# Kernel optimization log

Measured on AMD Instinct MI355X. Metric: run time of the kernel, lower is better.

## Reference

```python
import jax, jax.numpy as jnp
import numpy as np

EPS = 1e-6
NH, DK, DV = 4, 32, 32

def _ln2d(x, w, b):
    # LayerNorm2d: normalize over channel dim (dim=1), biased variance
    mu = jnp.mean(x, axis=1, keepdims=True)
    var = jnp.mean((x - mu) ** 2, axis=1, keepdims=True)
    y = (x - mu) / jnp.sqrt(var + EPS)
    return w[None, :, None, None] * y + b[None, :, None, None]

def _c1x1(w, x):
    # 1x1 conv == per-pixel matmul: w [out,in], x [B,C,H,W]
    return jnp.einsum('oc,bchw->bohw', w, x)

def _shifts(x, r):
    # All (2r+1)^2 zero-padded spatial shifts, row-major (dy,dx) like nn.Unfold.
    B, C, H, W = x.shape
    xp = jnp.pad(x, ((0, 0), (0, 0), (r, r), (r, r)))
    return jnp.stack([xp[:, :, dy:dy + H, dx:dx + W]
                      for dy in range(2 * r + 1) for dx in range(2 * r + 1)], axis=0)

def _local_attn(q, k, v, kernel):
    # Correlation-pyramid local attention: per-pixel q.k over kxk window of k,
    # softmax over window (temperature sqrt(d_k)), weighted sum of v window
    # (weights shared across channels, per ChannelAttention).
    B, _, H, W = q.shape
    r = (kernel - 1) // 2
    K2 = kernel * kernel
    qh = q.reshape(B, NH, DK, H, W)
    ks = _shifts(k, r).reshape(K2, B, NH, DK, H, W)
    corr = jnp.einsum('bncyx,jbncyx->jbnyx', qh, ks)            # [K2,B,NH,H,W]
    attn = jax.nn.softmax(corr / jnp.sqrt(jnp.float32(DK)), axis=0)
    vs = _shifts(v, r).reshape(K2, B, NH, DV, H, W)
    out = jnp.einsum('jbnyx,jbncyx->bncyx', attn, vs)
    return out.reshape(B, NH * DV, H, W)

def _mha(q, k, v, kernel, wq, wk, wv, fc, lnw, lnb):
    resid = q
    heads = _local_attn(_c1x1(wq, q), _c1x1(wk, k), _c1x1(wv, v), kernel)
    out = _c1x1(fc, heads) + resid   # residual BEFORE LN (per source)
    return _ln2d(out, lnw, lnb)

def _ffn(x, w1, b1, w2, b2, lnw, lnb):
    h = jax.nn.relu(_c1x1(w1, x) + b1[None, :, None, None])
    y = _c1x1(w2, h) + b2[None, :, None, None]
    return _ln2d(y, lnw, lnb) + x    # LN BEFORE residual add (per source)

def setup_inputs():
    key = jax.random.key(0)
    ks = jax.random.split(key, 24)
    B, C, H, W = 4, 128, 96, 96
    s = (2.0 / C) ** 0.5
    f = jnp.float32
    return {
        'input1': jax.random.normal(ks[0], (B, C, H, W), f),
        'input2': jax.random.normal(ks[1], (B, C, H, W), f),
        'wq_s': jax.random.normal(ks[2], (NH * DK, C), f) * s,
        'wk_s': jax.random.normal(ks[3], (NH * DK, C), f) * s,
        'wv_s': jax.random.normal(ks[4], (NH * DV, C), f) * s,
        'fc_s': jax.random.normal(ks[5], (C, NH * DV), f) * s,
        'lnw_s': jnp.ones((C,), f),
        'lnb_s': jnp.zeros((C,), f),
        'wq_c': jax.random.normal(ks[6], (NH * DK, C), f) * s,
        'wk_c': jax.random.normal(ks[7], (NH * DK, C), f) * s,
        'wv_c': jax.random.normal(ks[8], (NH * DV, C), f) * s,
        'fc_c': jax.random.normal(ks[9], (C, NH * DV), f) * s,
        'lnw_c': jnp.ones((C,), f),
        'lnb_c': jnp.zeros((C,), f),
        'w1': jax.random.normal(ks[10], (C, C), f) * s,
        'b1': jnp.zeros((C,), f),
        'w2': jax.random.normal(ks[11], (C, C), f) * s,
        'b2': jnp.zeros((C,), f),
        'lnw_f': jnp.ones((C,), f),
        'lnb_f': jnp.zeros((C,), f),
        'kernel': 5,
        'pad': 2,
    }

def reference(input1, input2, wq_s, wk_s, wv_s, fc_s, lnw_s, lnb_s,
              wq_c, wk_c, wv_c, fc_c, lnw_c, lnb_c,
              w1, b1, w2, b2, lnw_f, lnb_f, kernel, pad):
    slf1 = _mha(input1, input1, input1, kernel, wq_s, wk_s, wv_s, fc_s, lnw_s, lnb_s)
    slf2 = _mha(input2, input2, input2, kernel, wq_s, wk_s, wv_s, fc_s, lnw_s, lnb_s)
    crs1 = _mha(slf1, slf2, slf2, kernel, wq_c, wk_c, wv_c, fc_c, lnw_c, lnb_c)
    crs2 = _mha(slf2, slf1, slf1, kernel, wq_c, wk_c, wv_c, fc_c, lnw_c, lnb_c)
    out1 = _ffn(crs1, w1, b1, w2, b2, lnw_f, lnb_f)
    out2 = _ffn(crs2, w1, b1, w2, b2, lnw_f, lnb_f)
    return (out1, out2)
```

## Files before the change

kernel.cpp:

```cpp
#include <hip/hip_runtime.h>
#include <hip/hip_bf16.h>

typedef _Float16 h16;
typedef __attribute__((ext_vector_type(8))) _Float16 f16x8v;
typedef __attribute__((ext_vector_type(2))) _Float16 h2v;
typedef __attribute__((ext_vector_type(4))) float f32x4;
#define DI __device__ __forceinline__

constexpr int CH = 128;
constexpr int HH = 96, WW = 96;
constexpr int HW = HH * WW;
constexpr int NB = 4;
constexpr int NPIX = NB * HW;
constexpr int LDT = 136;
constexpr size_t HP = (size_t)NPIX * 32;
constexpr int GH = NPIX / 64;
constexpr int TY = 4, TX = 32;
constexpr int HYH = TY + 4, HXH = TX + 4;
constexpr int LDC = 40;
constexpr int ATB = NPIX / (TY * TX) * 4;

struct __attribute__((aligned(16))) h16x8 { h16 h[8]; };
struct Set { h16 *q, *k, *v; };

DI float h2f(h16 x) { return (float)x; }
DI h16   f2h(float x) { return (h16)x; }


DI void stage_x_cl(const h16* __restrict__ src, int ldx, h16* xl, int t) {
    #pragma unroll
    for (int i = 0; i < 4; ++i) {
        int id = t + 256 * i, px = id >> 4, cc = (id & 15) * 8;
        *reinterpret_cast<f16x8v*>(&xl[px * LDT + cc]) =
            *reinterpret_cast<const f16x8v*>(&src[(size_t)px * ldx + cc]);
    }
}

DI void stage_x_pl(const float* __restrict__ src, h16* xl, int t) {
    #pragma unroll
    for (int i = 0; i < 8; ++i) {
        int id = t + 256 * i, c = id >> 4, p4 = (id & 15) * 4;
        float4 v = *reinterpret_cast<const float4*>(&src[(size_t)c * HW + p4]);
        xl[(p4 + 0) * LDT + c] = f2h(v.x);
        xl[(p4 + 1) * LDT + c] = f2h(v.y);
        xl[(p4 + 2) * LDT + c] = f2h(v.z);
        xl[(p4 + 3) * LDT + c] = f2h(v.w);
    }
}

DI void stage_x_hm(const h16* __restrict__ Tq, h16* xl, int p0, int t) {
    const int px = t >> 2, c8 = (t & 3) * 8;
    #pragma unroll
    for (int h = 0; h < 4; ++h)
        *reinterpret_cast<f16x8v*>(&xl[px * LDT + h * 32 + c8]) =
            *reinterpret_cast<const f16x8v*>(&Tq[(size_t)h * HP + (size_t)(p0 + px) * 32 + c8]);
}

DI void stage_w(const float* __restrict__ w, h16* wl, int t) {
    #pragma unroll
    for (int i = 0; i < 8; ++i) {
        int id = t + 256 * i, o = id >> 4, cc = (id & 15) * 8;
        float4 a = *reinterpret_cast<const float4*>(&w[o * CH + cc]);
        float4 b = *reinterpret_cast<const float4*>(&w[o * CH + cc + 4]);
        h16x8 tmp;
        tmp.h[0] = f2h(a.x); tmp.h[1] = f2h(a.y); tmp.h[2] = f2h(a.z); tmp.h[3] = f2h(a.w);
        tmp.h[4] = f2h(b.x); tmp.h[5] = f2h(b.y); tmp.h[6] = f2h(b.z); tmp.h[7] = f2h(b.w);
        *reinterpret_cast<f16x8v*>(&wl[o * LDT + cc]) = *reinterpret_cast<const f16x8v*>(&tmp);
    }
}

DI void stage_r_pl(const float* __restrict__ src, float* rl, int t) {
    #pragma unroll
    for (int i = 0; i < 8; ++i) {
        int id = t + 256 * i, c = id >> 4, p4 = (id & 15) * 4;
        float4 v = *reinterpret_cast<const float4*>(&src[(size_t)c * HW + p4]);
        rl[c * 65 + p4 + 0] = v.x;
        rl[c * 65 + p4 + 1] = v.y;
        rl[c * 65 + p4 + 2] = v.z;
        rl[c * 65 + p4 + 3] = v.w;
    }
}

DI void gemm64(const h16* xl, const h16* wl, int w, int l, f32x4* acc) {
    const int s = l & 15, g = l >> 4;
    #pragma unroll
    for (int ks = 0; ks < 4; ++ks) {
        f16x8v a = *reinterpret_cast<const f16x8v*>(&xl[(16 * w + s) * LDT + ks * 32 + g * 8]);
        #pragma unroll
        for (int n = 0; n < 8; ++n) {
            f16x8v b = *reinterpret_cast<const f16x8v*>(&wl[(16 * n + s) * LDT + ks * 32 + g * 8]);
            acc[n] = __builtin_amdgcn_mfma_f32_16x16x32_f16(a, b, acc[n], 0, 0, 0);
        }
    }
}

DI void qkv_epi(const f32x4* acc, h16* comp, int p0, int w, int l) {
    const int s = l & 15, g = l >> 4;
    #pragma unroll
    for (int n = 0; n < 8; ++n) {
        const int o = 16 * n + s, head = o >> 5, ch = o & 31;
        h16* pl = comp + (size_t)head * HP;
        #pragma unroll
        for (int j = 0; j < 4; ++j) {
            int px = 16 * w + 4 * g + j;
            pl[(size_t)(p0 + px) * 32 + ch] = f2h(acc[n][j]);
        }
    }
}

DI void ln128(float r[8][4], const float* gm, const float* bt, float val[8][4]) {
    #pragma unroll
    for (int j = 0; j < 4; ++j) {
        float sm = 0.f, sq = 0.f;
        #pragma unroll
        for (int n = 0; n < 8; ++n) { float v = r[n][j]; sm += v; sq += v * v; }
        sm += __shfl_xor(sm, 1); sq += __shfl_xor(sq, 1);
        sm += __shfl_xor(sm, 2); sq += __shfl_xor(sq, 2);
        sm += __shfl_xor(sm, 4); sq += __shfl_xor(sq, 4);
        sm += __shfl_xor(sm, 8); sq += __shfl_xor(sq, 8);
        const float mu = sm * (1.f / 128.f);
        const float var = sq * (1.f / 128.f) - mu * mu;
        const float rs = rsqrtf(var + 1e-6f);
        #pragma unroll
        for (int n = 0; n < 8; ++n)
            val[n][j] = gm[n] * (r[n][j] - mu) * rs + bt[n];
    }
}

__global__ __launch_bounds__(256, 2)
void qkv_self_b(const float* __restrict__ x0, const float* __restrict__ x1,
                const float* __restrict__ w0, const float* __restrict__ w1_,
                const float* __restrict__ w2_, Set sA, Set sB) {
    __shared__ h16 xl[64 * LDT];
    __shared__ h16 wl[CH * LDT];
    const int bid = blockIdx.x, half = bid / GH, p0 = (bid % GH) * 64;
    const float* xv = half ? x1 : x0;
    Set S = half ? sB : sA;
    const int t = threadIdx.x;
    const int b = p0 / HW, hw0 = p0 % HW;
    stage_x_pl(xv + (size_t)b * CH * HW + hw0, xl, t);
    const int w = t >> 6, l = t & 63;
    #pragma unroll
    for (int m = 0; m < 3; ++m) {
        const float* wm = (m == 0) ? w0 : ((m == 1) ? w1_ : w2_);
        h16* comp = (m == 0) ? S.q : ((m == 1) ? S.k : S.v);
        __syncthreads();
        stage_w(wm, wl, t);
        __syncthreads();
        f32x4 acc[8];
        #pragma unroll
        for (int n = 0; n < 8; ++n) acc[n] = {0.f, 0.f, 0.f, 0.f};
        gemm64(xl, wl, w, l, acc);
        qkv_epi(acc, comp, p0, w, l);
    }
}

__global__ __launch_bounds__(256)
void attn5b(Set s0, Set s1) {
    __shared__ h16 kv[HYH * HXH * LDC];
    const int bid = blockIdx.x, setId = bid / ATB, id = bid - setId * ATB;
    Set S = setId ? s1 : s0;
    const int n = id & 3, tile = id >> 2;
    const int img = tile / 72, rem = tile % 72, tr = rem / 3, tc = rem % 3;
    const int y0 = tr * TY, x0 = tc * TX;
    const int t = threadIdx.x;
    const int p = t >> 1, half = t & 1, ch16 = half * 16;
    const int ty = p >> 5, tx = p & 31;
    h16* Qh = S.q + (size_t)n * HP;
    const h16* Kh = S.k + (size_t)n * HP;
    const h16* Vh = S.v + (size_t)n * HP;
    const int gp = img * HW + (y0 + ty) * WW + (x0 + tx);
    h16* qp = Qh + (size_t)gp * 32 + ch16;

    f16x8v q0 = *reinterpret_cast<const f16x8v*>(qp);
    f16x8v q1 = *reinterpret_cast<const f16x8v*>(qp + 8);
    {
        const h16 sc = (h16)0.17677669529663689f;
        #pragma unroll
        for (int e = 0; e < 8; ++e) { q0[e] *= sc; q1[e] *= sc; }
    }

    #pragma unroll
    for (int i = 0; i < 5; ++i) {
        int id2 = t + 256 * i;
        if (id2 < 1152) {
            int r = id2 / 144, c = id2 - r * 144, px = c >> 2, c8 = (c & 3) * 8;
            int y = y0 + r - 2, x = x0 + px - 2;
            f16x8v v = {0, 0, 0, 0, 0, 0, 0, 0};
            if ((unsigned)y < (unsigned)HH && (unsigned)x < (unsigned)WW)
                v = *reinterpret_cast<const f16x8v*>(&Kh[((size_t)(img * HW + y * WW + x)) * 32 + c8]);
            *reinterpret_cast<f16x8v*>(&kv[(r * HXH + px) * LDC + c8]) = v;
        }
    }
    __syncthreads();

    float corr[25];
    #pragma unroll
    for (int dy = 0; dy < 5; ++dy)
        #pragma unroll
        for (int dx = 0; dx < 5; ++dx) {
            const h16* kp = &kv[((ty + dy) * HXH + tx + dx) * LDC + ch16];
            f16x8v k0 = *reinterpret_cast<const f16x8v*>(kp);
            f16x8v k1 = *reinterpret_cast<const f16x8v*>(kp + 8);
            float s;
#if __has_builtin(__builtin_amdgcn_fdot2)
            s = __builtin_amdgcn_fdot2(h2v{q0[0], q0[1]}, h2v{k0[0], k0[1]}, 0.f, false);
            s = __builtin_amdgcn_fdot2(h2v{q0[2], q0[3]}, h2v{k0[2], k0[3]}, s, false);
            s = __builtin_amdgcn_fdot2(h2v{q0[4], q0[5]}, h2v{k0[4], k0[5]}, s, false);
            s = __builtin_amdgcn_fdot2(h2v{q0[6], q0[7]}, h2v{k0[6], k0[7]}, s, false);
            s = __builtin_amdgcn_fdot2(h2v{q1[0], q1[1]}, h2v{k1[0], k1[1]}, s, false);
            s = __builtin_amdgcn_fdot2(h2v{q1[2], q1[3]}, h2v{k1[2], k1[3]}, s, false);
            s = __builtin_amdgcn_fdot2(h2v{q1[4], q1[5]}, h2v{k1[4], k1[5]}, s, false);
            s = __builtin_amdgcn_fdot2(h2v{q1[6], q1[7]}, h2v{k1[6], k1[7]}, s, false);
#else
            s = 0.f;
            #pragma unroll
            for (int e = 0; e < 8; ++e) s += h2f(q0[e]) * h2f(k0[e]);
            #pragma unroll
            for (int e = 0; e < 8; ++e) s += h2f(q1[e]) * h2f(k1[e]);
#endif
            s += __shfl_xor(s, 1);
            corr[dy * 5 + dx] = s;
        }

    float m = corr[0];
    #pragma unroll
    for (int j = 1; j < 25; ++j) m = fmaxf(m, corr[j]);
    float sum = 0.f;
    #pragma unroll
    for (int j = 0; j < 25; ++j) {
        float e = __expf(corr[j] - m);
        corr[j] = e; sum += e;
    }
    const float inv = 1.f / sum;

    __syncthreads();
    #pragma unroll
    for (int i = 0; i < 5; ++i) {
        int id2 = t + 256 * i;
        if (id2 < 1152) {
            int r = id2 / 144, c = id2 - r * 144, px = c >> 2, c8 = (c & 3) * 8;
            int y = y0 + r - 2, x = x0 + px - 2;
            f16x8v v = {0, 0, 0, 0, 0, 0, 0, 0};
            if ((unsigned)y < (unsigned)HH && (unsigned)x < (unsigned)WW)
                v = *reinterpret_cast<const f16x8v*>(&Vh[((size_t)(img * HW + y * WW + x)) * 32 + c8]);
            *reinterpret_cast<f16x8v*>(&kv[(r * HXH + px) * LDC + c8]) = v;
        }
    }
    __syncthreads();

    f16x8v o0 = {0, 0, 0, 0, 0, 0, 0, 0};
    f16x8v o1 = {0, 0, 0, 0, 0, 0, 0, 0};
    #pragma unroll
    for (int dy = 0; dy < 5; ++dy)
        #pragma unroll
        for (int dx = 0; dx < 5; ++dx) {
            const h16 ah = f2h(corr[dy * 5 + dx]);
            const f16x8v av = {ah, ah, ah, ah, ah, ah, ah, ah};
            const h16* vp = &kv[((ty + dy) * HXH + tx + dx) * LDC + ch16];
            f16x8v v0 = *reinterpret_cast<const f16x8v*>(vp);
            f16x8v v1 = *reinterpret_cast<const f16x8v*>(vp + 8);
            o0 += av * v0;
            o1 += av * v1;
        }
    {
        const h16 ih = f2h(inv);
        const f16x8v iv = {ih, ih, ih, ih, ih, ih, ih, ih};
        o0 *= iv; o1 *= iv;
    }
    *reinterpret_cast<f16x8v*>(qp)     = o0;
    *reinterpret_cast<f16x8v*>(qp + 8) = o1;
}

__global__ __launch_bounds__(256, 2)
void fcx1_b(const h16* __restrict__ tA, const h16* __restrict__ tB,
            const float* __restrict__ in1, const float* __restrict__ in2,
            const float* __restrict__ wfc, const float* __restrict__ gamma,
            const float* __restrict__ beta,
            const float* __restrict__ wq, const float* __restrict__ wk,
            const float* __restrict__ wv,
            h16* __restrict__ x1g, h16* __restrict__ x2g, Set c1, Set c2) {
    __shared__ h16 xl[64 * LDT];
    __shared__ __align__(16) char wsm[CH * LDT * 2];
    h16*   wl = (h16*)wsm;
    float* rl = (float*)wsm;
    const int bid = blockIdx.x, half = bid / GH, p0 = (bid % GH) * 64;
    const h16*   tin = half ? tB : tA;
    const float* inr = half ? in2 : in1;
    h16*         xg  = half ? x2g : x1g;
    Set own   = half ? c2 : c1;
    Set other = half ? c1 : c2;
    const int t = threadIdx.x;
    const int w = t >> 6, l = t & 63, s = l & 15, g4 = l >> 4;
    const int b = p0 / HW, hw0 = p0 % HW;

    stage_x_hm(tin, xl, p0, t);
    stage_w(wfc, wl, t);
    __syncthreads();

    f32x4 accF[8];
    #pragma unroll
    for (int n = 0; n < 8; ++n) accF[n] = {0.f, 0.f, 0.f, 0.f};
    gemm64(xl, wl, w, l, accF);
    __syncthreads();

    stage_r_pl(inr + (size_t)b * CH * HW + hw0, rl, t);
    __syncthreads();

    h16 vX[8][4];
    {
        float gm[8], bt[8], r[8][4], val[8][4];
        #pragma unroll
        for (int n = 0; n < 8; ++n) { gm[n] = gamma[16 * n + s]; bt[n] = beta[16 * n + s]; }
        #pragma unroll
        for (int n = 0; n < 8; ++n) {
            const int o = 16 * n + s;
            #pragma unroll
            for (int j = 0; j < 4; ++j) {
                const int px = 16 * w + 4 * g4 + j;
                r[n][j] = accF[n][j] + rl[o * 65 + px];
            }
        }
        ln128(r, gm, bt, val);
        #pragma unroll
        for (int n = 0; n < 8; ++n)
            #pragma unroll
            for (int j = 0; j < 4; ++j) vX[n][j] = f2h(val[n][j]);
    }
    __syncthreads();
    #pragma unroll
    for (int n = 0; n < 8; ++n) {
        const int o = 16 * n + s;
        #pragma unroll
        for (int j = 0; j < 4; ++j) {
            const int px = 16 * w + 4 * g4 + j;
            xl[px * LDT + o] = vX[n][j];
            xg[(size_t)(p0 + px) * CH + o] = vX[n][j];
        }
    }
    stage_w(wq, wl, t);
    __syncthreads();
    {
        f32x4 acc[8];
        #pragma unroll
        for (int n = 0; n < 8; ++n) acc[n] = {0.f, 0.f, 0.f, 0.f};
        gemm64(xl, wl, w, l, acc);
        qkv_epi(acc, own.q, p0, w, l);
    }
    __syncthreads();
    stage_w(wk, wl, t);
    __syncthreads();
    {
        f32x4 acc[8];
        #pragma unroll
        for (int n = 0; n < 8; ++n) acc[n] = {0.f, 0.f, 0.f, 0.f};
        gemm64(xl, wl, w, l, acc);
        qkv_epi(acc, other.k, p0, w, l);
    }
    __syncthreads();
    stage_w(wv, wl, t);
    __syncthreads();
    {
        f32x4 acc[8];
        #pragma unroll
        for (int n = 0; n < 8; ++n) acc[n] = {0.f, 0.f, 0.f, 0.f};
        gemm64(xl, wl, w, l, acc);
        qkv_epi(acc, other.v, p0, w, l);
    }
}

__global__ __launch_bounds__(256, 2)
void ffn_ln_b(const h16* __restrict__ t0, const h16* __restrict__ t1,
              const h16* __restrict__ x0, const h16* __restrict__ x1,
              const float* __restrict__ wfc, const float* __restrict__ gc,
              const float* __restrict__ bc,
              const float* __restrict__ w1m, const float* __restrict__ b1v,
              const float* __restrict__ w2m, const float* __restrict__ b2v,
              const float* __restrict__ gf, const float* __restrict__ bf,
              float* __restrict__ o0, float* __restrict__ o1) {
    __shared__ __align__(16) char smem[64 * LDT * 2 * 2 + CH * LDT * 2];
    h16*   xl = (h16*)smem;
    h16*   yl = (h16*)(smem + 64 * LDT * 2);
    h16*   wl = (h16*)(smem + 64 * LDT * 2 * 2);
    float* ll = (float*)(smem + 64 * LDT * 2 * 2);
    const int bid = blockIdx.x, half = bid / GH, p0 = (bid % GH) * 64;
    const h16* tin = half ? t1 : t0;
    const h16* xg  = half ? x1 : x0;
    float* outp = half ? o1 : o0;
    const int t = threadIdx.x;
    const int w = t >> 6, l = t & 63, s = l & 15, g4 = l >> 4;

    stage_x_hm(tin, xl, p0, t);
    stage_w(wfc, wl, t);
    __syncthreads();

    h16 yv[8][4];
    {
        f32x4 acc[8];
        #pragma unroll
        for (int n = 0; n < 8; ++n) acc[n] = {0.f, 0.f, 0.f, 0.f};
        gemm64(xl, wl, w, l, acc);
        float gm[8], bt[8], r[8][4], val[8][4];
        #pragma unroll
        for (int n = 0; n < 8; ++n) { gm[n] = gc[16 * n + s]; bt[n] = bc[16 * n + s]; }
        #pragma unroll
        for (int n = 0; n < 8; ++n) {
            const int o = 16 * n + s;
            #pragma unroll
            for (int j = 0; j < 4; ++j) {
                const int px = 16 * w + 4 * g4 + j;
                r[n][j] = acc[n][j] + h2f(xg[(size_t)(p0 + px) * CH + o]);
            }
        }
        ln128(r, gm, bt, val);
        #pragma unroll
        for (int n = 0; n < 8; ++n)
            #pragma unroll
            for (int j = 0; j < 4; ++j) yv[n][j] = f2h(val[n][j]);
    }
    __syncthreads();
    #pragma unroll
    for (int n = 0; n < 8; ++n) {
        const int o = 16 * n + s;
        #pragma unroll
        for (int j = 0; j < 4; ++j)
            yl[(16 * w + 4 * g4 + j) * LDT + o] = yv[n][j];
    }
    stage_w(w1m, wl, t);
    __syncthreads();

    {
        f32x4 acc[8];
        #pragma unroll
        for (int n = 0; n < 8; ++n) acc[n] = {0.f, 0.f, 0.f, 0.f};
        gemm64(yl, wl, w, l, acc);
        #pragma unroll
        for (int n = 0; n < 8; ++n) {
            const int o = 16 * n + s;
            const float bv = b1v[o];
            #pragma unroll
            for (int j = 0; j < 4; ++j)
                xl[(16 * w + 4 * g4 + j) * LDT + o] = f2h(fmaxf(acc[n][j] + bv, 0.f));
        }
    }
    __syncthreads();
    stage_w(w2m, wl, t);
    __syncthreads();

    float val[8][4];
    {
        f32x4 acc[8];
        #pragma unroll
        for (int n = 0; n < 8; ++n) acc[n] = {0.f, 0.f, 0.f, 0.f};
        gemm64(xl, wl, w, l, acc);
        float gm[8], bt[8], r[8][4];
        #pragma unroll
        for (int n = 0; n < 8; ++n) { gm[n] = gf[16 * n + s]; bt[n] = bf[16 * n + s]; }
        #pragma unroll
        for (int n = 0; n < 8; ++n) {
            const int o = 16 * n + s;
            const float bv = b2v[o];
            #pragma unroll
            for (int j = 0; j < 4; ++j) r[n][j] = acc[n][j] + bv;
        }
        ln128(r, gm, bt, val);
        #pragma unroll
        for (int n = 0; n < 8; ++n) {
            const int o = 16 * n + s;
            #pragma unroll
            for (int j = 0; j < 4; ++j)
                val[n][j] += h2f(yl[(16 * w + 4 * g4 + j) * LDT + o]);
        }
    }
    __syncthreads();
    #pragma unroll
    for (int n = 0; n < 8; ++n) {
        const int o = 16 * n + s;
        #pragma unroll
        for (int j = 0; j < 4; ++j) ll[o * 65 + 16 * w + 4 * g4 + j] = val[n][j];
    }
    __syncthreads();
    const int b = p0 / HW, hw0 = p0 % HW;
    #pragma unroll
    for (int i = 0; i < 8; ++i) {
        int id = t + 256 * i, c = id >> 4, p4 = (id & 15) * 4;
        float4 v = { ll[c * 65 + p4], ll[c * 65 + p4 + 1],
                     ll[c * 65 + p4 + 2], ll[c * 65 + p4 + 3] };
        *reinterpret_cast<float4*>(&outp[(size_t)b * CH * HW + (size_t)c * HW + hw0 + p4]) = v;
    }
}

extern "C" void kernel_launch(void* const* d_in, const int* in_sizes, int n_in,
                              void* d_out, int out_size, void* d_ws, size_t ws_size,
                              hipStream_t stream) {
    (void)in_sizes; (void)n_in; (void)out_size; (void)ws_size;
    const float* in1  = (const float*)d_in[0];
    const float* in2  = (const float*)d_in[1];
    const float* wq_s = (const float*)d_in[2];
    const float* wk_s = (const float*)d_in[3];
    const float* wv_s = (const float*)d_in[4];
    const float* fc_s = (const float*)d_in[5];
    const float* lnw_s= (const float*)d_in[6];
    const float* lnb_s= (const float*)d_in[7];
    const float* wq_c = (const float*)d_in[8];
    const float* wk_c = (const float*)d_in[9];
    const float* wv_c = (const float*)d_in[10];
    const float* fc_c = (const float*)d_in[11];
    const float* lnw_c= (const float*)d_in[12];
    const float* lnb_c= (const float*)d_in[13];
    const float* w1   = (const float*)d_in[14];
    const float* b1   = (const float*)d_in[15];
    const float* w2   = (const float*)d_in[16];
    const float* b2   = (const float*)d_in[17];
    const float* lnw_f= (const float*)d_in[18];
    const float* lnb_f= (const float*)d_in[19];

    const size_t BUF  = (size_t)NPIX * CH;
    const size_t BUFB = BUF * 2;
    char* ws = (char*)d_ws;
    h16* W0 = (h16*)(ws + 0 * BUFB);
    h16* W1 = (h16*)(ws + 1 * BUFB);
    h16* W2 = (h16*)(ws + 2 * BUFB);
    h16* W3 = (h16*)(ws + 3 * BUFB);
    h16* D0 = (h16*)d_out;
    h16* D1 = (h16*)((char*)d_out + 1 * BUFB);
    h16* D2 = (h16*)((char*)d_out + 2 * BUFB);
    h16* D3 = (h16*)((char*)d_out + 3 * BUFB);
    float* out1 = (float*)d_out;
    float* out2 = (float*)d_out + BUF;

    const dim3 B(256);

    Set SA = {W0, D0, D1};
    Set SB = {W1, D2, D3};
    h16* X1 = W2;
    h16* X2 = W3;
    Set C1 = {W0, D0, D1};
    Set C2 = {W1, D2, D3};

    qkv_self_b<<<dim3(2 * GH), B, 0, stream>>>(in1, in2, wq_s, wk_s, wv_s, SA, SB);
    attn5b<<<dim3(2 * ATB), B, 0, stream>>>(SA, SB);
    fcx1_b<<<dim3(2 * GH), B, 0, stream>>>(SA.q, SB.q, in1, in2,
                                           fc_s, lnw_s, lnb_s,
                                           wq_c, wk_c, wv_c, X1, X2, C1, C2);
    attn5b<<<dim3(2 * ATB), B, 0, stream>>>(C1, C2);
    ffn_ln_b<<<dim3(2 * GH), B, 0, stream>>>(C1.q, C2.q, X1, X2,
                                             fc_c, lnw_c, lnb_c,
                                             w1, b1, w2, b2, lnw_f, lnb_f,
                                             out1, out2);
}
```

Baseline: 153.4 us.

## Split GEMM kernels across 8 waves with cross-wave LayerNorm reduction

The three 1x1-conv GEMM kernels go from 256 to 512 threads. Each wave now computes half of the output channels for 16 pixels instead of all 128. LayerNorm statistics are reduced across the two channel-half waves through small shared arrays, which adds an extra barrier. The goal is more waves per block to hide latency and lower register pressure, at the cost of duplicated A-fragment loads and added synchronisation.

```diff
diff --git a/kernel.cpp b/kernel.cpp
--- a/kernel.cpp
+++ b/kernel.cpp
@@ -27,19 +27,10 @@
 DI h16   f2h(float x) { return (h16)x; }
 
 
-DI void stage_x_cl(const h16* __restrict__ src, int ldx, h16* xl, int t) {
+DI void stage_x_pl512(const float* __restrict__ src, h16* xl, int t) {
     #pragma unroll
     for (int i = 0; i < 4; ++i) {
-        int id = t + 256 * i, px = id >> 4, cc = (id & 15) * 8;
-        *reinterpret_cast<f16x8v*>(&xl[px * LDT + cc]) =
-            *reinterpret_cast<const f16x8v*>(&src[(size_t)px * ldx + cc]);
-    }
-}
-
-DI void stage_x_pl(const float* __restrict__ src, h16* xl, int t) {
-    #pragma unroll
-    for (int i = 0; i < 8; ++i) {
-        int id = t + 256 * i, c = id >> 4, p4 = (id & 15) * 4;
+        int id = t + 512 * i, c = id >> 4, p4 = (id & 15) * 4;
         float4 v = *reinterpret_cast<const float4*>(&src[(size_t)c * HW + p4]);
         xl[(p4 + 0) * LDT + c] = f2h(v.x);
         xl[(p4 + 1) * LDT + c] = f2h(v.y);
@@ -48,18 +39,20 @@
     }
 }
 
-DI void stage_x_hm(const h16* __restrict__ Tq, h16* xl, int p0, int t) {
-    const int px = t >> 2, c8 = (t & 3) * 8;
-    #pragma unroll
-    for (int h = 0; h < 4; ++h)
+DI void stage_x_hm512(const h16* __restrict__ Tq, h16* xl, int p0, int t) {
+    #pragma unroll
+    for (int i = 0; i < 2; ++i) {
+        int id = t + 512 * i;
+        int px = id >> 4, q = id & 15, h = q >> 2, c8 = (q & 3) * 8;
         *reinterpret_cast<f16x8v*>(&xl[px * LDT + h * 32 + c8]) =
             *reinterpret_cast<const f16x8v*>(&Tq[(size_t)h * HP + (size_t)(p0 + px) * 32 + c8]);
-}
-
-DI void stage_w(const float* __restrict__ w, h16* wl, int t) {
-    #pragma unroll
-    for (int i = 0; i < 8; ++i) {
-        int id = t + 256 * i, o = id >> 4, cc = (id & 15) * 8;
+    }
+}
+
+DI void stage_w512(const float* __restrict__ w, h16* wl, int t) {
+    #pragma unroll
+    for (int i = 0; i < 4; ++i) {
+        int id = t + 512 * i, o = id >> 4, cc = (id & 15) * 8;
         float4 a = *reinterpret_cast<const float4*>(&w[o * CH + cc]);
         float4 b = *reinterpret_cast<const float4*>(&w[o * CH + cc + 4]);
         h16x8 tmp;
@@ -69,10 +62,10 @@
     }
 }
 
-DI void stage_r_pl(const float* __restrict__ src, float* rl, int t) {
-    #pragma unroll
-    for (int i = 0; i < 8; ++i) {
-        int id = t + 256 * i, c = id >> 4, p4 = (id & 15) * 4;
+DI void stage_r_pl512(const float* __restrict__ src, float* rl, int t) {
+    #pragma unroll
+    for (int i = 0; i < 4; ++i) {
+        int id = t + 512 * i, c = id >> 4, p4 = (id & 15) * 4;
         float4 v = *reinterpret_cast<const float4*>(&src[(size_t)c * HW + p4]);
         rl[c * 65 + p4 + 0] = v.x;
         rl[c * 65 + p4 + 1] = v.y;
@@ -81,53 +74,35 @@
     }
 }
 
-DI void gemm64(const h16* xl, const h16* wl, int w, int l, f32x4* acc) {
+DI void gemm64h(const h16* xl, const h16* wl, int wp, int wo, int l, f32x4* acc) {
     const int s = l & 15, g = l >> 4;
     #pragma unroll
     for (int ks = 0; ks < 4; ++ks) {
-        f16x8v a = *reinterpret_cast<const f16x8v*>(&xl[(16 * w + s) * LDT + ks * 32 + g * 8]);
-        #pragma unroll
-        for (int n = 0; n < 8; ++n) {
-            f16x8v b = *reinterpret_cast<const f16x8v*>(&wl[(16 * n + s) * LDT + ks * 32 + g * 8]);
+        f16x8v a = *reinterpret_cast<const f16x8v*>(&xl[(16 * wp + s) * LDT + ks * 32 + g * 8]);
+        #pragma unroll
+        for (int n = 0; n < 4; ++n) {
+            f16x8v b = *reinterpret_cast<const f16x8v*>(
+                &wl[(16 * (4 * wo + n) + s) * LDT + ks * 32 + g * 8]);
             acc[n] = __builtin_amdgcn_mfma_f32_16x16x32_f16(a, b, acc[n], 0, 0, 0);
         }
     }
 }
 
-DI void qkv_epi(const f32x4* acc, h16* comp, int p0, int w, int l) {
+DI void qkv_epi_h(const f32x4* acc, h16* comp, int p0, int wp, int wo, int l) {
     const int s = l & 15, g = l >> 4;
     #pragma unroll
-    for (int n = 0; n < 8; ++n) {
-        const int o = 16 * n + s, head = o >> 5, ch = o & 31;
+    for (int n = 0; n < 4; ++n) {
+        const int o = 64 * wo + 16 * n + s, head = o >> 5, ch = o & 31;
         h16* pl = comp + (size_t)head * HP;
         #pragma unroll
         for (int j = 0; j < 4; ++j) {
-            int px = 16 * w + 4 * g + j;
+            int px = 16 * wp + 4 * g + j;
             pl[(size_t)(p0 + px) * 32 + ch] = f2h(acc[n][j]);
         }
     }
 }
 
-DI void ln128(float r[8][4], const float* gm, const float* bt, float val[8][4]) {
-    #pragma unroll
-    for (int j = 0; j < 4; ++j) {
-        float sm = 0.f, sq = 0.f;
-        #pragma unroll
-        for (int n = 0; n < 8; ++n) { float v = r[n][j]; sm += v; sq += v * v; }
-        sm += __shfl_xor(sm, 1); sq += __shfl_xor(sq, 1);
-        sm += __shfl_xor(sm, 2); sq += __shfl_xor(sq, 2);
-        sm += __shfl_xor(sm, 4); sq += __shfl_xor(sq, 4);
-        sm += __shfl_xor(sm, 8); sq += __shfl_xor(sq, 8);
-        const float mu = sm * (1.f / 128.f);
-        const float var = sq * (1.f / 128.f) - mu * mu;
-        const float rs = rsqrtf(var + 1e-6f);
-        #pragma unroll
-        for (int n = 0; n < 8; ++n)
-            val[n][j] = gm[n] * (r[n][j] - mu) * rs + bt[n];
-    }
-}
-
-__global__ __launch_bounds__(256, 2)
+__global__ __launch_bounds__(512, 2)
 void qkv_self_b(const float* __restrict__ x0, const float* __restrict__ x1,
                 const float* __restrict__ w0, const float* __restrict__ w1_,
                 const float* __restrict__ w2_, Set sA, Set sB) {
@@ -138,20 +113,20 @@
     Set S = half ? sB : sA;
     const int t = threadIdx.x;
     const int b = p0 / HW, hw0 = p0 % HW;
-    stage_x_pl(xv + (size_t)b * CH * HW + hw0, xl, t);
-    const int w = t >> 6, l = t & 63;
+    stage_x_pl512(xv + (size_t)b * CH * HW + hw0, xl, t);
+    const int w8 = t >> 6, l = t & 63, wp = w8 & 3, wo = w8 >> 2;
     #pragma unroll
     for (int m = 0; m < 3; ++m) {
         const float* wm = (m == 0) ? w0 : ((m == 1) ? w1_ : w2_);
         h16* comp = (m == 0) ? S.q : ((m == 1) ? S.k : S.v);
         __syncthreads();
-        stage_w(wm, wl, t);
+        stage_w512(wm, wl, t);
         __syncthreads();
-        f32x4 acc[8];
-        #pragma unroll
-        for (int n = 0; n < 8; ++n) acc[n] = {0.f, 0.f, 0.f, 0.f};
-        gemm64(xl, wl, w, l, acc);
-        qkv_epi(acc, comp, p0, w, l);
+        f32x4 acc[4];
+        #pragma unroll
+        for (int n = 0; n < 4; ++n) acc[n] = {0.f, 0.f, 0.f, 0.f};
+        gemm64h(xl, wl, wp, wo, l, acc);
+        qkv_epi_h(acc, comp, p0, wp, wo, l);
     }
 }
 
@@ -272,7 +247,7 @@
     *reinterpret_cast<f16x8v*>(qp + 8) = o1;
 }
 
-__global__ __launch_bounds__(256, 2)
+__global__ __launch_bounds__(512, 2)
 void fcx1_b(const h16* __restrict__ tA, const h16* __restrict__ tB,
             const float* __restrict__ in1, const float* __restrict__ in2,
             const float* __restrict__ wfc, const float* __restrict__ gamma,
@@ -282,6 +257,7 @@
             h16* __restrict__ x1g, h16* __restrict__ x2g, Set c1, Set c2) {
     __shared__ h16 xl[64 * LDT];
     __shared__ __align__(16) char wsm[CH * LDT * 2];
+    __shared__ float redS[128], redQ[128];
     h16*   wl = (h16*)wsm;
     float* rl = (float*)wsm;
     const int bid = blockIdx.x, half = bid / GH, p0 = (bid % GH) * 64;
@@ -291,85 +267,109 @@
     Set own   = half ? c2 : c1;
     Set other = half ? c1 : c2;
     const int t = threadIdx.x;
-    const int w = t >> 6, l = t & 63, s = l & 15, g4 = l >> 4;
+    const int w8 = t >> 6, l = t & 63, s = l & 15, g4 = l >> 4;
+    const int wp = w8 & 3, wo = w8 >> 2;
     const int b = p0 / HW, hw0 = p0 % HW;
 
-    stage_x_hm(tin, xl, p0, t);
-    stage_w(wfc, wl, t);
-    __syncthreads();
-
-    f32x4 accF[8];
-    #pragma unroll
-    for (int n = 0; n < 8; ++n) accF[n] = {0.f, 0.f, 0.f, 0.f};
-    gemm64(xl, wl, w, l, accF);
-    __syncthreads();
-
-    stage_r_pl(inr + (size_t)b * CH * HW + hw0, rl, t);
-    __syncthreads();
-
-    h16 vX[8][4];
-    {
-        float gm[8], bt[8], r[8][4], val[8][4];
-        #pragma unroll
-        for (int n = 0; n < 8; ++n) { gm[n] = gamma[16 * n + s]; bt[n] = beta[16 * n + s]; }
-        #pragma unroll
-        for (int n = 0; n < 8; ++n) {
-            const int o = 16 * n + s;
-            #pragma unroll
-            for (int j = 0; j < 4; ++j) {
-                const int px = 16 * w + 4 * g4 + j;
-                r[n][j] = accF[n][j] + rl[o * 65 + px];
-            }
-        }
-        ln128(r, gm, bt, val);
-        #pragma unroll
-        for (int n = 0; n < 8; ++n)
-            #pragma unroll
-            for (int j = 0; j < 4; ++j) vX[n][j] = f2h(val[n][j]);
-    }
-    __syncthreads();
-    #pragma unroll
-    for (int n = 0; n < 8; ++n) {
-        const int o = 16 * n + s;
+    stage_x_hm512(tin, xl, p0, t);
+    stage_w512(wfc, wl, t);
+    __syncthreads();
+
+    f32x4 accF[4];
+    #pragma unroll
+    for (int n = 0; n < 4; ++n) accF[n] = {0.f, 0.f, 0.f, 0.f};
+    gemm64h(xl, wl, wp, wo, l, accF);
+    __syncthreads();
+
+    stage_r_pl512(inr + (size_t)b * CH * HW + hw0, rl, t);
+    __syncthreads();
+
+    float gm[4], bt[4], r[4][4];
+    #pragma unroll
+    for (int n = 0; n < 4; ++n) {
+        const int o = 64 * wo + 16 * n + s;
+        gm[n] = gamma[o]; bt[n] = beta[o];
+        #pragma unroll
+        for (int j = 0; j < 4; ++j)
+            r[n][j] = accF[n][j] + rl[o * 65 + (16 * wp + 4 * g4 + j)];
+    }
+    float smA[4], sqA[4];
+    #pragma unroll
+    for (int j = 0; j < 4; ++j) {
+        float sm = 0.f, sq = 0.f;
+        #pragma unroll
+        for (int n = 0; n < 4; ++n) { float v = r[n][j]; sm += v; sq += v * v; }
+        sm += __shfl_xor(sm, 1); sq += __shfl_xor(sq, 1);
+        sm += __shfl_xor(sm, 2); sq += __shfl_xor(sq, 2);
+        sm += __shfl_xor(sm, 4); sq += __shfl_xor(sq, 4);
+        sm += __shfl_xor(sm, 8); sq += __shfl_xor(sq, 8);
+        smA[j] = sm; sqA[j] = sq;
+    }
+    if (s == 0) {
         #pragma unroll
         for (int j = 0; j < 4; ++j) {
-            const int px = 16 * w + 4 * g4 + j;
+            const int px = 16 * wp + 4 * g4 + j;
+            redS[px * 2 + wo] = smA[j];
+            redQ[px * 2 + wo] = sqA[j];
+        }
+    }
+    __syncthreads();
+
+    h16 vX[4][4];
+    #pragma unroll
+    for (int j = 0; j < 4; ++j) {
+        const int px = 16 * wp + 4 * g4 + j;
+        const float smT = redS[px * 2] + redS[px * 2 + 1];
+        const float sqT = redQ[px * 2] + redQ[px * 2 + 1];
+        const float mu = smT * (1.f / 128.f);
+        const float var = sqT * (1.f / 128.f) - mu * mu;
+        const float rs = rsqrtf(var + 1e-6f);
+        #pragma unroll
+        for (int n = 0; n < 4; ++n)
+            vX[n][j] = f2h(gm[n] * (r[n][j] - mu) * rs + bt[n]);
+    }
+    #pragma unroll
+    for (int n = 0; n < 4; ++n) {
+        const int o = 64 * wo + 16 * n + s;
+        #pragma unroll
+        for (int j = 0; j < 4; ++j) {
+            const int px = 16 * wp + 4 * g4 + j;
             xl[px * LDT + o] = vX[n][j];
             xg[(size_t)(p0 + px) * CH + o] = vX[n][j];
         }
     }
-    stage_w(wq, wl, t);
-    __syncthreads();
-    {
-        f32x4 acc[8];
-        #pragma unroll
-        for (int n = 0; n < 8; ++n) acc[n] = {0.f, 0.f, 0.f, 0.f};
-        gemm64(xl, wl, w, l, acc);
-        qkv_epi(acc, own.q, p0, w, l);
-    }
-    __syncthreads();
-    stage_w(wk, wl, t);
-    __syncthreads();
-    {
-        f32x4 acc[8];
-        #pragma unroll
-        for (int n = 0; n < 8; ++n) acc[n] = {0.f, 0.f, 0.f, 0.f};
-        gemm64(xl, wl, w, l, acc);
-        qkv_epi(acc, other.k, p0, w, l);
-    }
-    __syncthreads();
-    stage_w(wv, wl, t);
-    __syncthreads();
-    {
-        f32x4 acc[8];
-        #pragma unroll
-        for (int n = 0; n < 8; ++n) acc[n] = {0.f, 0.f, 0.f, 0.f};
-        gemm64(xl, wl, w, l, acc);
-        qkv_epi(acc, other.v, p0, w, l);
-    }
-}
-
-__global__ __launch_bounds__(256, 2)
+    stage_w512(wq, wl, t);
+    __syncthreads();
+    {
+        f32x4 acc[4];
+        #pragma unroll
+        for (int n = 0; n < 4; ++n) acc[n] = {0.f, 0.f, 0.f, 0.f};
+        gemm64h(xl, wl, wp, wo, l, acc);
+        qkv_epi_h(acc, own.q, p0, wp, wo, l);
+    }
+    __syncthreads();
+    stage_w512(wk, wl, t);
+    __syncthreads();
+    {
+        f32x4 acc[4];
+        #pragma unroll
+        for (int n = 0; n < 4; ++n) acc[n] = {0.f, 0.f, 0.f, 0.f};
+        gemm64h(xl, wl, wp, wo, l, acc);
+        qkv_epi_h(acc, other.k, p0, wp, wo, l);
+    }
+    __syncthreads();
+    stage_w512(wv, wl, t);
+    __syncthreads();
+    {
+        f32x4 acc[4];
+        #pragma unroll
+        for (int n = 0; n < 4; ++n) acc[n] = {0.f, 0.f, 0.f, 0.f};
+        gemm64h(xl, wl, wp, wo, l, acc);
+        qkv_epi_h(acc, other.v, p0, wp, wo, l);
+    }
+}
+
+__global__ __launch_bounds__(512, 2)
 void ffn_ln_b(const h16* __restrict__ t0, const h16* __restrict__ t1,
               const h16* __restrict__ x0, const h16* __restrict__ x1,
               const float* __restrict__ wfc, const float* __restrict__ gc,
@@ -379,6 +379,7 @@
               const float* __restrict__ gf, const float* __restrict__ bf,
               float* __restrict__ o0, float* __restrict__ o1) {
     __shared__ __align__(16) char smem[64 * LDT * 2 * 2 + CH * LDT * 2];
+    __shared__ float redS[128], redQ[128];
     h16*   xl = (h16*)smem;
     h16*   yl = (h16*)(smem + 64 * LDT * 2);
     h16*   wl = (h16*)(smem + 64 * LDT * 2 * 2);
@@ -388,102 +389,143 @@
     const h16* xg  = half ? x1 : x0;
     float* outp = half ? o1 : o0;
     const int t = threadIdx.x;
-    const int w = t >> 6, l = t & 63, s = l & 15, g4 = l >> 4;
-
-    stage_x_hm(tin, xl, p0, t);
-    stage_w(wfc, wl, t);
-    __syncthreads();
-
-    h16 yv[8][4];
-    {
-        f32x4 acc[8];
-        #pragma unroll
-        for (int n = 0; n < 8; ++n) acc[n] = {0.f, 0.f, 0.f, 0.f};
-        gemm64(xl, wl, w, l, acc);
-        float gm[8], bt[8], r[8][4], val[8][4];
-        #pragma unroll
-        for (int n = 0; n < 8; ++n) { gm[n] = gc[16 * n + s]; bt[n] = bc[16 * n + s]; }
-        #pragma unroll
-        for (int n = 0; n < 8; ++n) {
-            const int o = 16 * n + s;
+    const int w8 = t >> 6, l = t & 63, s = l & 15, g4 = l >> 4;
+    const int wp = w8 & 3, wo = w8 >> 2;
+
+    stage_x_hm512(tin, xl, p0, t);
+    stage_w512(wfc, wl, t);
+    __syncthreads();
+
+    float r[4][4];
+    {
+        f32x4 acc[4];
+        #pragma unroll
+        for (int n = 0; n < 4; ++n) acc[n] = {0.f, 0.f, 0.f, 0.f};
+        gemm64h(xl, wl, wp, wo, l, acc);
+        #pragma unroll
+        for (int n = 0; n < 4; ++n) {
+            const int o = 64 * wo + 16 * n + s;
             #pragma unroll
             for (int j = 0; j < 4; ++j) {
-                const int px = 16 * w + 4 * g4 + j;
+                const int px = 16 * wp + 4 * g4 + j;
                 r[n][j] = acc[n][j] + h2f(xg[(size_t)(p0 + px) * CH + o]);
             }
         }
-        ln128(r, gm, bt, val);
-        #pragma unroll
-        for (int n = 0; n < 8; ++n)
-            #pragma unroll
-            for (int j = 0; j < 4; ++j) yv[n][j] = f2h(val[n][j]);
-    }
-    __syncthreads();
-    #pragma unroll
-    for (int n = 0; n < 8; ++n) {
-        const int o = 16 * n + s;
-        #pragma unroll
-        for (int j = 0; j < 4; ++j)
-            yl[(16 * w + 4 * g4 + j) * LDT + o] = yv[n][j];
-    }
-    stage_w(w1m, wl, t);
-    __syncthreads();
-
-    {
-        f32x4 acc[8];
-        #pragma unroll
-        for (int n = 0; n < 8; ++n) acc[n] = {0.f, 0.f, 0.f, 0.f};
-        gemm64(yl, wl, w, l, acc);
-        #pragma unroll
-        for (int n = 0; n < 8; ++n) {
-            const int o = 16 * n + s;
+    }
+    {
+        float smA[4], sqA[4];
+        #pragma unroll
+        for (int j = 0; j < 4; ++j) {
+            float sm = 0.f, sq = 0.f;
+            #pragma unroll
+            for (int n = 0; n < 4; ++n) { float v = r[n][j]; sm += v; sq += v * v; }
+            sm += __shfl_xor(sm, 1); sq += __shfl_xor(sq, 1);
+            sm += __shfl_xor(sm, 2); sq += __shfl_xor(sq, 2);
+            sm += __shfl_xor(sm, 4); sq += __shfl_xor(sq, 4);
+            sm += __shfl_xor(sm, 8); sq += __shfl_xor(sq, 8);
+            smA[j] = sm; sqA[j] = sq;
+        }
+        if (s == 0) {
+            #pragma unroll
+            for (int j = 0; j < 4; ++j) {
+                const int px = 16 * wp + 4 * g4 + j;
+                redS[px * 2 + wo] = smA[j];
+                redQ[px * 2 + wo] = sqA[j];
+            }
+        }
+    }
+    __syncthreads();
+    #pragma unroll
+    for (int j = 0; j < 4; ++j) {
+        const int px = 16 * wp + 4 * g4 + j;
+        const float smT = redS[px * 2] + redS[px * 2 + 1];
+        const float sqT = redQ[px * 2] + redQ[px * 2 + 1];
+        const float mu = smT * (1.f / 128.f);
+        const float var = sqT * (1.f / 128.f) - mu * mu;
+        const float rs = rsqrtf(var + 1e-6f);
+        #pragma unroll
+        for (int n = 0; n < 4; ++n) {
+            const int o = 64 * wo + 16 * n + s;
+            yl[px * LDT + o] = f2h(gc[o] * (r[n][j] - mu) * rs + bc[o]);
+        }
+    }
+    stage_w512(w1m, wl, t);
+    __syncthreads();
+
+    {
+        f32x4 acc[4];
+        #pragma unroll
+        for (int n = 0; n < 4; ++n) acc[n] = {0.f, 0.f, 0.f, 0.f};
+        gemm64h(yl, wl, wp, wo, l, acc);
+        #pragma unroll
+        for (int n = 0; n < 4; ++n) {
+            const int o = 64 * wo + 16 * n + s;
             const float bv = b1v[o];
             #pragma unroll
             for (int j = 0; j < 4; ++j)
-                xl[(16 * w + 4 * g4 + j) * LDT + o] = f2h(fmaxf(acc[n][j] + bv, 0.f));
-        }
-    }
-    __syncthreads();
-    stage_w(w2m, wl, t);
-    __syncthreads();
-
-    float val[8][4];
-    {
-        f32x4 acc[8];
-        #pragma unroll
-        for (int n = 0; n < 8; ++n) acc[n] = {0.f, 0.f, 0.f, 0.f};
-        gemm64(xl, wl, w, l, acc);
-        float gm[8], bt[8], r[8][4];
-        #pragma unroll
-        for (int n = 0; n < 8; ++n) { gm[n] = gf[16 * n + s]; bt[n] = bf[16 * n + s]; }
-        #pragma unroll
-        for (int n = 0; n < 8; ++n) {
-            const int o = 16 * n + s;
+                xl[(16 * wp + 4 * g4 + j) * LDT + o] = f2h(fmaxf(acc[n][j] + bv, 0.f));
+        }
+    }
+    __syncthreads();
+    stage_w512(w2m, wl, t);
+    __syncthreads();
+
+    float r2[4][4];
+    {
+        f32x4 acc[4];
+        #pragma unroll
+        for (int n = 0; n < 4; ++n) acc[n] = {0.f, 0.f, 0.f, 0.f};
+        gemm64h(xl, wl, wp, wo, l, acc);
+        #pragma unroll
+        for (int n = 0; n < 4; ++n) {
+            const int o = 64 * wo + 16 * n + s;
             const float bv = b2v[o];
             #pragma unroll
-            for (int j = 0; j < 4; ++j) r[n][j] = acc[n][j] + bv;
-        }
-        ln128(r, gm, bt, val);
-        #pragma unroll
-        for (int n = 0; n < 8; ++n) {
-            const int o = 16 * n + s;
-            #pragma unroll
-            for (int j = 0; j < 4; ++j)
-                val[n][j] += h2f(yl[(16 * w + 4 * g4 + j) * LDT + o]);
-        }
-    }
-    __syncthreads();
-    #pragma unroll
-    for (int n = 0; n < 8; ++n) {
-        const int o = 16 * n + s;
-        #pragma unroll
-        for (int j = 0; j < 4; ++j) ll[o * 65 + 16 * w + 4 * g4 + j] = val[n][j];
+            for (int j = 0; j < 4; ++j) r2[n][j] = acc[n][j] + bv;
+        }
+        float smA[4], sqA[4];
+        #pragma unroll
+        for (int j = 0; j < 4; ++j) {
+            float sm = 0.f, sq = 0.f;
+            #pragma unroll
+            for (int n = 0; n < 4; ++n) { float v = r2[n][j]; sm += v; sq += v * v; }
+            sm += __shfl_xor(sm, 1); sq += __shfl_xor(sq, 1);
+            sm += __shfl_xor(sm, 2); sq += __shfl_xor(sq, 2);
+            sm += __shfl_xor(sm, 4); sq += __shfl_xor(sq, 4);
+            sm += __shfl_xor(sm, 8); sq += __shfl_xor(sq, 8);
+            smA[j] = sm; sqA[j] = sq;
+        }
+        if (s == 0) {
+            #pragma unroll
+            for (int j = 0; j < 4; ++j) {
+                const int px = 16 * wp + 4 * g4 + j;
+                redS[px * 2 + wo] = smA[j];
+                redQ[px * 2 + wo] = sqA[j];
+            }
+        }
+    }
+    __syncthreads();
+    #pragma unroll
+    for (int j = 0; j < 4; ++j) {
+        const int px = 16 * wp + 4 * g4 + j;
+        const float smT = redS[px * 2] + redS[px * 2 + 1];
+        const float sqT = redQ[px * 2] + redQ[px * 2 + 1];
+        const float mu = smT * (1.f / 128.f);
+        const float var = sqT * (1.f / 128.f) - mu * mu;
+        const float rs = rsqrtf(var + 1e-6f);
+        #pragma unroll
+        for (int n = 0; n < 4; ++n) {
+            const int o = 64 * wo + 16 * n + s;
+            const float v = gf[o] * (r2[n][j] - mu) * rs + bf[o]
+                          + h2f(yl[px * LDT + o]);
+            ll[o * 65 + px] = v;
+        }
     }
     __syncthreads();
     const int b = p0 / HW, hw0 = p0 % HW;
     #pragma unroll
-    for (int i = 0; i < 8; ++i) {
-        int id = t + 256 * i, c = id >> 4, p4 = (id & 15) * 4;
+    for (int i = 0; i < 4; ++i) {
+        int id = t + 512 * i, c = id >> 4, p4 = (id & 15) * 4;
         float4 v = { ll[c * 65 + p4], ll[c * 65 + p4 + 1],
                      ll[c * 65 + p4 + 2], ll[c * 65 + p4 + 3] };
         *reinterpret_cast<float4*>(&outp[(size_t)b * CH * HW + (size_t)c * HW + hw0 + p4]) = v;
@@ -529,7 +571,7 @@
     float* out1 = (float*)d_out;
     float* out2 = (float*)d_out + BUF;
 
-    const dim3 B(256);
+    const dim3 B2(512), BA(256);
 
     Set SA = {W0, D0, D1};
     Set SB = {W1, D2, D3};
@@ -538,14 +580,14 @@
     Set C1 = {W0, D0, D1};
     Set C2 = {W1, D2, D3};
 
-    qkv_self_b<<<dim3(2 * GH), B, 0, stream>>>(in1, in2, wq_s, wk_s, wv_s, SA, SB);
-    attn5b<<<dim3(2 * ATB), B, 0, stream>>>(SA, SB);
-    fcx1_b<<<dim3(2 * GH), B, 0, stream>>>(SA.q, SB.q, in1, in2,
-                                           fc_s, lnw_s, lnb_s,
-                                           wq_c, wk_c, wv_c, X1, X2, C1, C2);
-    attn5b<<<dim3(2 * ATB), B, 0, stream>>>(C1, C2);
-    ffn_ln_b<<<dim3(2 * GH), B, 0, stream>>>(C1.q, C2.q, X1, X2,
-                                             fc_c, lnw_c, lnb_c,
-                                             w1, b1, w2, b2, lnw_f, lnb_f,
-                                             out1, out2);
-}
+    qkv_self_b<<<dim3(2 * GH), B2, 0, stream>>>(in1, in2, wq_s, wk_s, wv_s, SA, SB);
+    attn5b<<<dim3(2 * ATB), BA, 0, stream>>>(SA, SB);
+    fcx1_b<<<dim3(2 * GH), B2, 0, stream>>>(SA.q, SB.q, in1, in2,
+                                            fc_s, lnw_s, lnb_s,
+                                            wq_c, wk_c, wv_c, X1, X2, C1, C2);
+    attn5b<<<dim3(2 * ATB), BA, 0, stream>>>(C1, C2);
+    ffn_ln_b<<<dim3(2 * GH), B2, 0, stream>>>(C1.q, C2.q, X1, X2,
+                                              fc_c, lnw_c, lnb_c,
+                                              w1, b1, w2, b2, lnw_f, lnb_f,
+                                              out1, out2);
+}
```

New measurement: 155.1 us. No clear change (+1.1%).
